# Optimization experiments

Hardware: AMD Instinct MI355X
Metric: run time of the kernel (lower is better)

## Reference

```python
import jax, jax.numpy as jnp
import numpy as np

B, S, D, H = 4, 2048, 1024, 16
HD = D // H  # head_dim = 64


def setup_inputs() -> dict:
    key = jax.random.key(0)
    ks = jax.random.split(key, 9)
    s = 1.0 / np.sqrt(D)
    return {
        "x": jax.random.normal(ks[0], (B, S, D), dtype=jnp.float32),
        "wq": jax.random.uniform(ks[1], (D, D), jnp.float32, -s, s),
        "bq": jax.random.uniform(ks[2], (D,), jnp.float32, -s, s),
        "wk": jax.random.uniform(ks[3], (D, D), jnp.float32, -s, s),
        "bk": jax.random.uniform(ks[4], (D,), jnp.float32, -s, s),
        "wv": jax.random.uniform(ks[5], (D, D), jnp.float32, -s, s),
        "bv": jax.random.uniform(ks[6], (D,), jnp.float32, -s, s),
        "wo": jax.random.uniform(ks[7], (D, D), jnp.float32, -s, s),
        "bo": jax.random.uniform(ks[8], (D,), jnp.float32, -s, s),
    }


def reference(x, wq, bq, wk, bk, wv, bv, wo, bo):
    b, s, _ = x.shape
    # projections (torch Linear: y = x @ W.T + b)
    q = (x @ wq.T + bq).reshape(b, s, H, HD).transpose(0, 2, 1, 3)  # [B,H,S,HD]
    k = (x @ wk.T + bk).reshape(b, s, H, HD).transpose(0, 2, 1, 3)
    v = (x @ wv.T + bv).reshape(b, s, H, HD).transpose(0, 2, 1, 3)
    scores = jnp.einsum("bhqd,bhkd->bhqk", q, k) / jnp.sqrt(jnp.float32(HD))
    attn = jax.nn.softmax(scores, axis=-1)  # full [B,H,S,S] as in original
    ctx = jnp.einsum("bhqk,bhkd->bhqd", attn, v)
    ctx = ctx.transpose(0, 2, 1, 3).reshape(b, s, D)
    return ctx @ wo.T + bo
```

## Files before the change

kernel.cpp:

```cpp
#include <hip/hip_runtime.h>
#include <stdint.h>


typedef __bf16 bf16x8 __attribute__((ext_vector_type(8)));
typedef float f32x4 __attribute__((ext_vector_type(4)));
typedef float f32x16 __attribute__((ext_vector_type(16)));

__device__ __forceinline__ uint16_t f2bf(float f) {
  union { float f; uint32_t u; } c;
  c.f = f;
  uint32_t u = c.u + 0x7fffu + ((c.u >> 16) & 1u);
  return (uint16_t)(u >> 16);
}

__device__ __forceinline__ float exp2_hw(float x) {
#if defined(__has_builtin) && __has_builtin(__builtin_amdgcn_exp2f)
  return __builtin_amdgcn_exp2f(x);
#else
  return exp2f(x);
#endif
}

__device__ __forceinline__ uint32_t cvt_pk_bf16(float lo, float hi) {
  uint32_t r;
  asm("v_cvt_pk_bf16_f32 %0, %1, %2" : "=v"(r) : "v"(lo), "v"(hi));
  return r;
}

__device__ __forceinline__ void gload16(const void* g, void* l) {
  __builtin_amdgcn_global_load_lds(
      (const __attribute__((address_space(1))) uint32_t*)g,
      (__attribute__((address_space(3))) uint32_t*)l,
      16, 0, 0);
}

__global__ void cvt_f32_bf16(const float* __restrict__ in,
                             uint16_t* __restrict__ out, int n4) {
  int i = blockIdx.x * blockDim.x + threadIdx.x;
  if (i >= n4) return;
  float4 v = reinterpret_cast<const float4*>(in)[i];
  union { uint16_t u[4]; uint2 d; } o;
  o.u[0] = f2bf(v.x); o.u[1] = f2bf(v.y);
  o.u[2] = f2bf(v.z); o.u[3] = f2bf(v.w);
  reinterpret_cast<uint2*>(out)[i] = o.d;
}

template <int MODE>
__global__ __launch_bounds__(256, 2)
void gemm_nt(const uint16_t* __restrict__ A,
             const uint16_t* __restrict__ W0, const uint16_t* __restrict__ W1,
             const uint16_t* __restrict__ W2,
             const float* __restrict__ b0, const float* __restrict__ b1,
             const float* __restrict__ b2,
             uint16_t* __restrict__ oq, uint16_t* __restrict__ ok2,
             uint16_t* __restrict__ ovT, float* __restrict__ ofp) {
  __shared__ __align__(16) uint16_t Alds[2][128 * 32];
  __shared__ __align__(16) uint16_t Blds[2][128 * 32];

  const int tid = threadIdx.x;
  const int w = tid >> 6;
  const int l = tid & 63;
  const int wm = w >> 1, wn = w & 1;
  const int g = l >> 4, c16 = l & 15;
  const int brow = blockIdx.y * 128;
  const int bcol = blockIdx.x * 128;

  const uint16_t* Wsel = W0;
  const float* bsel = b0;
  if (MODE == 0) {
    const int which = bcol >> 10;
    Wsel = (which == 0) ? W0 : ((which == 1) ? W1 : W2);
    bsel = (which == 0) ? b0 : ((which == 1) ? b1 : b2);
  }
  const int bw = bcol & 1023;

  const int srow = l >> 2;
  const int scol = (l & 3) * 8;

  f32x4 acc[4][4];
#pragma unroll
  for (int i = 0; i < 4; ++i)
#pragma unroll
    for (int j = 0; j < 4; ++j) acc[i][j] = {0.f, 0.f, 0.f, 0.f};

#pragma unroll
  for (int i2 = 0; i2 < 2; ++i2) {
    const int c = 2 * w + i2;
    gload16(A + (size_t)(brow + c * 16 + srow) * 1024 + scol, &Alds[0][c * 512]);
    gload16(Wsel + (size_t)(bw + c * 16 + srow) * 1024 + scol, &Blds[0][c * 512]);
  }

  for (int kt = 0; kt < 32; ++kt) {
    __syncthreads();
    const int cur = kt & 1;
    if (kt + 1 < 32) {
      const int k0 = (kt + 1) * 32;
#pragma unroll
      for (int i2 = 0; i2 < 2; ++i2) {
        const int c = 2 * w + i2;
        gload16(A + (size_t)(brow + c * 16 + srow) * 1024 + k0 + scol,
                &Alds[cur ^ 1][c * 512]);
        gload16(Wsel + (size_t)(bw + c * 16 + srow) * 1024 + k0 + scol,
                &Blds[cur ^ 1][c * 512]);
      }
    }
    bf16x8 af[4], bfr[4];
#pragma unroll
    for (int i = 0; i < 4; ++i)
      af[i] = *reinterpret_cast<const bf16x8*>(
          &Alds[cur][(wm * 64 + i * 16 + c16) * 32 + g * 8]);
#pragma unroll
    for (int j = 0; j < 4; ++j)
      bfr[j] = *reinterpret_cast<const bf16x8*>(
          &Blds[cur][(wn * 64 + j * 16 + c16) * 32 + g * 8]);
#pragma unroll
    for (int i = 0; i < 4; ++i)
#pragma unroll
      for (int j = 0; j < 4; ++j)
        acc[i][j] = __builtin_amdgcn_mfma_f32_16x16x32_bf16(af[i], bfr[j],
                                                            acc[i][j], 0, 0, 0);
  }

#pragma unroll
  for (int i = 0; i < 4; ++i) {
#pragma unroll
    for (int j = 0; j < 4; ++j) {
      const int n = bcol + wn * 64 + j * 16 + c16;
      const int nn = n & 1023;
      const float bias = bsel[nn];
#pragma unroll
      for (int r = 0; r < 4; ++r) {
        const int m = brow + wm * 64 + i * 16 + g * 4 + r;
        const float val = acc[i][j][r] + bias;
        if (MODE == 0) {
          const int which = n >> 10;
          const int s = m & 2047, b = m >> 11;
          const int h = nn >> 6, hd = nn & 63;
          const size_t bh = (size_t)(b * 16 + h);
          if (which == 0)
            oq[(bh * 2048 + s) * 64 + hd] = f2bf(val * 0.18033688011112042f);
          else if (which == 1)
            ok2[(bh * 2048 + s) * 64 + hd] = f2bf(val);
          else
            ovT[(bh * 64 + hd) * 2048 + s] = f2bf(val);
        } else {
          ofp[(size_t)m * 1024 + n] = val;
        }
      }
    }
  }
}

__global__ __launch_bounds__(256, 2)
void attn_fwd(const uint16_t* __restrict__ Q, const uint16_t* __restrict__ K,
              const uint16_t* __restrict__ VT, uint16_t* __restrict__ CTX) {
  __shared__ __align__(16) uint16_t Klds[2][64 * 64];
  __shared__ __align__(16) uint16_t Vlds[2][64 * 64];

  const int tid = threadIdx.x;
  const int w = tid >> 6;
  const int l = tid & 63;
  const int hi = l >> 5, q5 = l & 31;
  const int bh = blockIdx.x;
  const int qb = blockIdx.y;
  const int qrow_base = qb * 256 + w * 64;

  const int kappa = (q5 & 3) | (((q5 >> 3) & 1) << 2) | (((q5 >> 2) & 1) << 3) |
                    ((q5 >> 4) << 4);

  bf16x8 qf[2][4];
#pragma unroll
  for (int grp = 0; grp < 2; ++grp) {
    const uint16_t* qp =
        Q + ((size_t)bh * 2048 + qrow_base + grp * 32 + q5) * 64 + 8 * hi;
#pragma unroll
    for (int ks = 0; ks < 4; ++ks)
      qf[grp][ks] = *reinterpret_cast<const bf16x8*>(qp + 16 * ks);
  }

  f32x16 ctx[2][2];
#pragma unroll
  for (int grp = 0; grp < 2; ++grp)
#pragma unroll
    for (int hb = 0; hb < 2; ++hb)
#pragma unroll
      for (int e = 0; e < 16; ++e) ctx[grp][hb][e] = 0.f;
  float M[2] = {-1024.0f, -1024.0f};
  float L[2] = {0.f, 0.f};

  auto stage = [&](int kt, int buf) {
#pragma unroll
    for (int i2 = 0; i2 < 2; ++i2) {
      const int c = 2 * w + i2;
      const int lb = c * 1024 + l * 16;
      const int row = lb >> 7;
      const int so = lb ^ ((row & 7) << 4);
      const int colel = (so & 127) >> 1;
      gload16(K + ((size_t)bh * 2048 + kt * 64 + row) * 64 + colel,
              &Klds[buf][c * 512]);
      gload16(VT + ((size_t)bh * 64 + row) * 2048 + kt * 64 + colel,
              &Vlds[buf][c * 512]);
    }
  };

  int koff[4], voff[2][2];
#pragma unroll
  for (int ks = 0; ks < 4; ++ks)
    koff[ks] = (32 * ks + 16 * hi) ^ ((kappa & 7) << 4);
#pragma unroll
  for (int half = 0; half < 2; ++half)
#pragma unroll
    for (int ks2 = 0; ks2 < 2; ++ks2)
      voff[half][ks2] = (half * 64 + 32 * ks2 + 16 * hi) ^ ((q5 & 7) << 4);

  stage(0, 0);

  for (int kt = 0; kt < 32; ++kt) {
    __syncthreads();
    const int cur = kt & 1;
    if (kt + 1 < 32) stage(kt + 1, cur ^ 1);
    const uint8_t* kb = reinterpret_cast<const uint8_t*>(&Klds[cur][0]);
    const uint8_t* vb = reinterpret_cast<const uint8_t*>(&Vlds[cur][0]);

#pragma unroll
    for (int half = 0; half < 2; ++half) {
      bf16x8 kf[4];
      const int krow = half * 32 + kappa;
#pragma unroll
      for (int ks = 0; ks < 4; ++ks)
        kf[ks] = *reinterpret_cast<const bf16x8*>(kb + krow * 128 + koff[ks]);
      bf16x8 vf[2][2];
#pragma unroll
      for (int hb = 0; hb < 2; ++hb) {
        const int vrow = 32 * hb + q5;
#pragma unroll
        for (int ks2 = 0; ks2 < 2; ++ks2)
          vf[hb][ks2] = *reinterpret_cast<const bf16x8*>(
              vb + vrow * 128 + voff[half][ks2]);
      }

#pragma unroll
      for (int grp = 0; grp < 2; ++grp) {
        const float negM = -M[grp];
        f32x16 sc;
#pragma unroll
        for (int e = 0; e < 16; ++e) sc[e] = negM;
        __builtin_amdgcn_s_setprio(1);
#pragma unroll
        for (int ks = 0; ks < 4; ++ks)
          sc = __builtin_amdgcn_mfma_f32_32x32x16_bf16(kf[ks], qf[grp][ks], sc,
                                                       0, 0, 0);
        __builtin_amdgcn_s_setprio(0);

        float m0 = fmaxf(fmaxf(sc[0], sc[1]), fmaxf(sc[2], sc[3]));
        float m1 = fmaxf(fmaxf(sc[4], sc[5]), fmaxf(sc[6], sc[7]));
        float m2 = fmaxf(fmaxf(sc[8], sc[9]), fmaxf(sc[10], sc[11]));
        float m3 = fmaxf(fmaxf(sc[12], sc[13]), fmaxf(sc[14], sc[15]));
        float mloc = fmaxf(fmaxf(m0, m1), fmaxf(m2, m3));
        mloc = fmaxf(mloc, __shfl_xor(mloc, 32));

        float p[16];
        if (__any(mloc > 8.0f)) {
          const float delta = fmaxf(mloc, 0.0f);
          const float corr = exp2_hw(-delta);
          M[grp] += delta;
          L[grp] *= corr;
#pragma unroll
          for (int hb = 0; hb < 2; ++hb)
#pragma unroll
            for (int e = 0; e < 16; ++e) ctx[grp][hb][e] *= corr;
#pragma unroll
          for (int e = 0; e < 16; ++e) p[e] = exp2_hw(sc[e] - delta);
        } else {
#pragma unroll
          for (int e = 0; e < 16; ++e) p[e] = exp2_hw(sc[e]);
        }

        L[grp] += ((p[0] + p[1]) + (p[2] + p[3])) +
                  ((p[4] + p[5]) + (p[6] + p[7])) +
                  ((p[8] + p[9]) + (p[10] + p[11])) +
                  ((p[12] + p[13]) + (p[14] + p[15]));

        union { uint32_t u[4]; bf16x8 v; } pa0, pa1;
        pa0.u[0] = cvt_pk_bf16(p[0], p[1]);
        pa0.u[1] = cvt_pk_bf16(p[2], p[3]);
        pa0.u[2] = cvt_pk_bf16(p[4], p[5]);
        pa0.u[3] = cvt_pk_bf16(p[6], p[7]);
        pa1.u[0] = cvt_pk_bf16(p[8], p[9]);
        pa1.u[1] = cvt_pk_bf16(p[10], p[11]);
        pa1.u[2] = cvt_pk_bf16(p[12], p[13]);
        pa1.u[3] = cvt_pk_bf16(p[14], p[15]);

        __builtin_amdgcn_s_setprio(1);
#pragma unroll
        for (int hb = 0; hb < 2; ++hb) {
          ctx[grp][hb] = __builtin_amdgcn_mfma_f32_32x32x16_bf16(
              vf[hb][0], pa0.v, ctx[grp][hb], 0, 0, 0);
          ctx[grp][hb] = __builtin_amdgcn_mfma_f32_32x32x16_bf16(
              vf[hb][1], pa1.v, ctx[grp][hb], 0, 0, 0);
        }
        __builtin_amdgcn_s_setprio(0);
      }
    }
  }

  const int b = bh >> 4, h = bh & 15;
#pragma unroll
  for (int grp = 0; grp < 2; ++grp) {
    float Lt = L[grp] + __shfl_xor(L[grp], 32);
    const float inv = 1.0f / Lt;
    const int s = qrow_base + grp * 32 + q5;
#pragma unroll
    for (int hb = 0; hb < 2; ++hb) {
#pragma unroll
      for (int t = 0; t < 4; ++t) {
        uint2 st;
        st.x = cvt_pk_bf16(ctx[grp][hb][4 * t] * inv,
                           ctx[grp][hb][4 * t + 1] * inv);
        st.y = cvt_pk_bf16(ctx[grp][hb][4 * t + 2] * inv,
                           ctx[grp][hb][4 * t + 3] * inv);
        *reinterpret_cast<uint2*>(
            &CTX[((size_t)b * 2048 + s) * 1024 + h * 64 + hb * 32 + t * 8 +
                 hi * 4]) = st;
      }
    }
  }
}

extern "C" void kernel_launch(void* const* d_in, const int* in_sizes, int n_in,
                              void* d_out, int out_size, void* d_ws,
                              size_t ws_size, hipStream_t stream) {
  (void)in_sizes; (void)n_in; (void)out_size; (void)ws_size;
  const float* x = (const float*)d_in[0];
  const float* wq = (const float*)d_in[1];
  const float* bq = (const float*)d_in[2];
  const float* wk = (const float*)d_in[3];
  const float* bk = (const float*)d_in[4];
  const float* wv = (const float*)d_in[5];
  const float* bv = (const float*)d_in[6];
  const float* wo = (const float*)d_in[7];
  const float* bo = (const float*)d_in[8];
  float* out = (float*)d_out;

  uint8_t* ws = (uint8_t*)d_ws;
  uint16_t* xb   = (uint16_t*)(ws + 0);
  uint16_t* wqb  = (uint16_t*)(ws + 16777216);
  uint16_t* wkb  = (uint16_t*)(ws + 16777216 + 2097152);
  uint16_t* wvb  = (uint16_t*)(ws + 16777216 + 2 * 2097152);
  uint16_t* wob  = (uint16_t*)(ws + 16777216 + 3 * 2097152);
  uint16_t* qws  = (uint16_t*)(ws + 25165824);
  uint16_t* kws  = (uint16_t*)(ws + 25165824 + 16777216);
  uint16_t* vtws = (uint16_t*)(ws + 25165824 + 2 * 16777216);
  uint16_t* ctxw = (uint16_t*)(ws + 25165824 + 3 * 16777216);

  cvt_f32_bf16<<<8192, 256, 0, stream>>>(x, xb, 2097152);
  cvt_f32_bf16<<<1024, 256, 0, stream>>>(wq, wqb, 262144);
  cvt_f32_bf16<<<1024, 256, 0, stream>>>(wk, wkb, 262144);
  cvt_f32_bf16<<<1024, 256, 0, stream>>>(wv, wvb, 262144);
  cvt_f32_bf16<<<1024, 256, 0, stream>>>(wo, wob, 262144);

  gemm_nt<0><<<dim3(24, 64), 256, 0, stream>>>(
      xb, wqb, wkb, wvb, bq, bk, bv, qws, kws, vtws, nullptr);
  attn_fwd<<<dim3(64, 8), 256, 0, stream>>>(qws, kws, vtws, ctxw);
  gemm_nt<1><<<dim3(8, 64), 256, 0, stream>>>(
      ctxw, wob, nullptr, nullptr, bo, nullptr, nullptr, nullptr, nullptr,
      nullptr, out);
}
```

Baseline: 234.8 us.

## Process full 64-key tile per query group with one softmax rescale

Reorders the attention inner loop so each query group computes scores for both 32-key halves before a single max/rescale/exp step, instead of per half. This halves the number of max reductions, cross-lane shuffles, __any checks and potential ctx rescales per tile, and keeps the negated running max in a persistent vector instead of re-broadcasting it. The cost is more live registers (two score tiles plus extra P fragments) and K/V fragments reloaded from LDS per group rather than shared across groups, which could raise LDS traffic or pressure occupancy.

```diff
diff --git a/kernel.cpp b/kernel.cpp
--- a/kernel.cpp
+++ b/kernel.cpp
@@ -187,6 +187,11 @@
       for (int e = 0; e < 16; ++e) ctx[grp][hb][e] = 0.f;
   float M[2] = {-1024.0f, -1024.0f};
   float L[2] = {0.f, 0.f};
+  f32x16 negMv[2];
+#pragma unroll
+  for (int grp = 0; grp < 2; ++grp)
+#pragma unroll
+    for (int e = 0; e < 16; ++e) negMv[grp][e] = 1024.0f;
 
   auto stage = [&](int kt, int buf) {
 #pragma unroll
@@ -223,84 +228,134 @@
     const uint8_t* vb = reinterpret_cast<const uint8_t*>(&Vlds[cur][0]);
 
 #pragma unroll
-    for (int half = 0; half < 2; ++half) {
-      bf16x8 kf[4];
-      const int krow = half * 32 + kappa;
-#pragma unroll
-      for (int ks = 0; ks < 4; ++ks)
-        kf[ks] = *reinterpret_cast<const bf16x8*>(kb + krow * 128 + koff[ks]);
-      bf16x8 vf[2][2];
+    for (int grp = 0; grp < 2; ++grp) {
+      f32x16 scA, scB;
+      {
+        bf16x8 kf[4];
+#pragma unroll
+        for (int ks = 0; ks < 4; ++ks)
+          kf[ks] = *reinterpret_cast<const bf16x8*>(
+              kb + kappa * 128 + koff[ks]);
+        __builtin_amdgcn_s_setprio(1);
+        scA = __builtin_amdgcn_mfma_f32_32x32x16_bf16(kf[0], qf[grp][0],
+                                                      negMv[grp], 0, 0, 0);
+        scA = __builtin_amdgcn_mfma_f32_32x32x16_bf16(kf[1], qf[grp][1], scA,
+                                                      0, 0, 0);
+        scA = __builtin_amdgcn_mfma_f32_32x32x16_bf16(kf[2], qf[grp][2], scA,
+                                                      0, 0, 0);
+        scA = __builtin_amdgcn_mfma_f32_32x32x16_bf16(kf[3], qf[grp][3], scA,
+                                                      0, 0, 0);
+        __builtin_amdgcn_s_setprio(0);
+      }
+      {
+        bf16x8 kf[4];
+        const int krow = 32 + kappa;
+#pragma unroll
+        for (int ks = 0; ks < 4; ++ks)
+          kf[ks] = *reinterpret_cast<const bf16x8*>(
+              kb + krow * 128 + koff[ks]);
+        __builtin_amdgcn_s_setprio(1);
+        scB = __builtin_amdgcn_mfma_f32_32x32x16_bf16(kf[0], qf[grp][0],
+                                                      negMv[grp], 0, 0, 0);
+        scB = __builtin_amdgcn_mfma_f32_32x32x16_bf16(kf[1], qf[grp][1], scB,
+                                                      0, 0, 0);
+        scB = __builtin_amdgcn_mfma_f32_32x32x16_bf16(kf[2], qf[grp][2], scB,
+                                                      0, 0, 0);
+        scB = __builtin_amdgcn_mfma_f32_32x32x16_bf16(kf[3], qf[grp][3], scB,
+                                                      0, 0, 0);
+        __builtin_amdgcn_s_setprio(0);
+      }
+
+      float a0 = fmaxf(fmaxf(scA[0], scA[1]), scA[2]);
+      float a1 = fmaxf(fmaxf(scA[3], scA[4]), scA[5]);
+      float a2 = fmaxf(fmaxf(scA[6], scA[7]), scA[8]);
+      float a3 = fmaxf(fmaxf(scA[9], scA[10]), scA[11]);
+      float a4 = fmaxf(fmaxf(scA[12], scA[13]), scA[14]);
+      float b0 = fmaxf(fmaxf(scB[0], scB[1]), scB[2]);
+      float b1 = fmaxf(fmaxf(scB[3], scB[4]), scB[5]);
+      float b2 = fmaxf(fmaxf(scB[6], scB[7]), scB[8]);
+      float b3 = fmaxf(fmaxf(scB[9], scB[10]), scB[11]);
+      float b4 = fmaxf(fmaxf(scB[12], scB[13]), scB[14]);
+      float t0 = fmaxf(fmaxf(a0, a1), a2);
+      float t1 = fmaxf(fmaxf(a3, a4), scA[15]);
+      float t2 = fmaxf(fmaxf(b0, b1), b2);
+      float t3 = fmaxf(fmaxf(b3, b4), scB[15]);
+      float mloc = fmaxf(fmaxf(t0, t1), fmaxf(t2, t3));
+      mloc = fmaxf(mloc, __shfl_xor(mloc, 32));
+
+      float pA[16], pB[16];
+      if (__any(mloc > 8.0f)) {
+        const float delta = fmaxf(mloc, 0.0f);
+        const float corr = exp2_hw(-delta);
+        M[grp] += delta;
+        const float nM = -M[grp];
+#pragma unroll
+        for (int e = 0; e < 16; ++e) negMv[grp][e] = nM;
+        L[grp] *= corr;
+#pragma unroll
+        for (int hb = 0; hb < 2; ++hb)
+#pragma unroll
+          for (int e = 0; e < 16; ++e) ctx[grp][hb][e] *= corr;
+#pragma unroll
+        for (int e = 0; e < 16; ++e) pA[e] = exp2_hw(scA[e] - delta);
+#pragma unroll
+        for (int e = 0; e < 16; ++e) pB[e] = exp2_hw(scB[e] - delta);
+      } else {
+#pragma unroll
+        for (int e = 0; e < 16; ++e) pA[e] = exp2_hw(scA[e]);
+#pragma unroll
+        for (int e = 0; e < 16; ++e) pB[e] = exp2_hw(scB[e]);
+      }
+
+      L[grp] += ((((pA[0] + pA[1]) + (pA[2] + pA[3])) +
+                  ((pA[4] + pA[5]) + (pA[6] + pA[7]))) +
+                 (((pA[8] + pA[9]) + (pA[10] + pA[11])) +
+                  ((pA[12] + pA[13]) + (pA[14] + pA[15])))) +
+                ((((pB[0] + pB[1]) + (pB[2] + pB[3])) +
+                  ((pB[4] + pB[5]) + (pB[6] + pB[7]))) +
+                 (((pB[8] + pB[9]) + (pB[10] + pB[11])) +
+                  ((pB[12] + pB[13]) + (pB[14] + pB[15]))));
+
+      union { uint32_t u[4]; bf16x8 v; } paA0, paA1, paB0, paB1;
+      paA0.u[0] = cvt_pk_bf16(pA[0], pA[1]);
+      paA0.u[1] = cvt_pk_bf16(pA[2], pA[3]);
+      paA0.u[2] = cvt_pk_bf16(pA[4], pA[5]);
+      paA0.u[3] = cvt_pk_bf16(pA[6], pA[7]);
+      paA1.u[0] = cvt_pk_bf16(pA[8], pA[9]);
+      paA1.u[1] = cvt_pk_bf16(pA[10], pA[11]);
+      paA1.u[2] = cvt_pk_bf16(pA[12], pA[13]);
+      paA1.u[3] = cvt_pk_bf16(pA[14], pA[15]);
+      paB0.u[0] = cvt_pk_bf16(pB[0], pB[1]);
+      paB0.u[1] = cvt_pk_bf16(pB[2], pB[3]);
+      paB0.u[2] = cvt_pk_bf16(pB[4], pB[5]);
+      paB0.u[3] = cvt_pk_bf16(pB[6], pB[7]);
+      paB1.u[0] = cvt_pk_bf16(pB[8], pB[9]);
+      paB1.u[1] = cvt_pk_bf16(pB[10], pB[11]);
+      paB1.u[2] = cvt_pk_bf16(pB[12], pB[13]);
+      paB1.u[3] = cvt_pk_bf16(pB[14], pB[15]);
+
+      __builtin_amdgcn_s_setprio(1);
 #pragma unroll
       for (int hb = 0; hb < 2; ++hb) {
         const int vrow = 32 * hb + q5;
-#pragma unroll
-        for (int ks2 = 0; ks2 < 2; ++ks2)
-          vf[hb][ks2] = *reinterpret_cast<const bf16x8*>(
-              vb + vrow * 128 + voff[half][ks2]);
-      }
-
-#pragma unroll
-      for (int grp = 0; grp < 2; ++grp) {
-        const float negM = -M[grp];
-        f32x16 sc;
-#pragma unroll
-        for (int e = 0; e < 16; ++e) sc[e] = negM;
-        __builtin_amdgcn_s_setprio(1);
-#pragma unroll
-        for (int ks = 0; ks < 4; ++ks)
-          sc = __builtin_amdgcn_mfma_f32_32x32x16_bf16(kf[ks], qf[grp][ks], sc,
-                                                       0, 0, 0);
-        __builtin_amdgcn_s_setprio(0);
-
-        float m0 = fmaxf(fmaxf(sc[0], sc[1]), fmaxf(sc[2], sc[3]));
-        float m1 = fmaxf(fmaxf(sc[4], sc[5]), fmaxf(sc[6], sc[7]));
-        float m2 = fmaxf(fmaxf(sc[8], sc[9]), fmaxf(sc[10], sc[11]));
-        float m3 = fmaxf(fmaxf(sc[12], sc[13]), fmaxf(sc[14], sc[15]));
-        float mloc = fmaxf(fmaxf(m0, m1), fmaxf(m2, m3));
-        mloc = fmaxf(mloc, __shfl_xor(mloc, 32));
-
-        float p[16];
-        if (__any(mloc > 8.0f)) {
-          const float delta = fmaxf(mloc, 0.0f);
-          const float corr = exp2_hw(-delta);
-          M[grp] += delta;
-          L[grp] *= corr;
-#pragma unroll
-          for (int hb = 0; hb < 2; ++hb)
-#pragma unroll
-            for (int e = 0; e < 16; ++e) ctx[grp][hb][e] *= corr;
-#pragma unroll
-          for (int e = 0; e < 16; ++e) p[e] = exp2_hw(sc[e] - delta);
-        } else {
-#pragma unroll
-          for (int e = 0; e < 16; ++e) p[e] = exp2_hw(sc[e]);
-        }
-
-        L[grp] += ((p[0] + p[1]) + (p[2] + p[3])) +
-                  ((p[4] + p[5]) + (p[6] + p[7])) +
-                  ((p[8] + p[9]) + (p[10] + p[11])) +
-                  ((p[12] + p[13]) + (p[14] + p[15]));
-
-        union { uint32_t u[4]; bf16x8 v; } pa0, pa1;
-        pa0.u[0] = cvt_pk_bf16(p[0], p[1]);
-        pa0.u[1] = cvt_pk_bf16(p[2], p[3]);
-        pa0.u[2] = cvt_pk_bf16(p[4], p[5]);
-        pa0.u[3] = cvt_pk_bf16(p[6], p[7]);
-        pa1.u[0] = cvt_pk_bf16(p[8], p[9]);
-        pa1.u[1] = cvt_pk_bf16(p[10], p[11]);
-        pa1.u[2] = cvt_pk_bf16(p[12], p[13]);
-        pa1.u[3] = cvt_pk_bf16(p[14], p[15]);
-
-        __builtin_amdgcn_s_setprio(1);
-#pragma unroll
-        for (int hb = 0; hb < 2; ++hb) {
-          ctx[grp][hb] = __builtin_amdgcn_mfma_f32_32x32x16_bf16(
-              vf[hb][0], pa0.v, ctx[grp][hb], 0, 0, 0);
-          ctx[grp][hb] = __builtin_amdgcn_mfma_f32_32x32x16_bf16(
-              vf[hb][1], pa1.v, ctx[grp][hb], 0, 0, 0);
-        }
-        __builtin_amdgcn_s_setprio(0);
-      }
+        const bf16x8 vA0 = *reinterpret_cast<const bf16x8*>(
+            vb + vrow * 128 + voff[0][0]);
+        const bf16x8 vA1 = *reinterpret_cast<const bf16x8*>(
+            vb + vrow * 128 + voff[0][1]);
+        const bf16x8 vB0 = *reinterpret_cast<const bf16x8*>(
+            vb + vrow * 128 + voff[1][0]);
+        const bf16x8 vB1 = *reinterpret_cast<const bf16x8*>(
+            vb + vrow * 128 + voff[1][1]);
+        ctx[grp][hb] = __builtin_amdgcn_mfma_f32_32x32x16_bf16(
+            vA0, paA0.v, ctx[grp][hb], 0, 0, 0);
+        ctx[grp][hb] = __builtin_amdgcn_mfma_f32_32x32x16_bf16(
+            vA1, paA1.v, ctx[grp][hb], 0, 0, 0);
+        ctx[grp][hb] = __builtin_amdgcn_mfma_f32_32x32x16_bf16(
+            vB0, paB0.v, ctx[grp][hb], 0, 0, 0);
+        ctx[grp][hb] = __builtin_amdgcn_mfma_f32_32x32x16_bf16(
+            vB1, paB1.v, ctx[grp][hb], 0, 0, 0);
+      }
+      __builtin_amdgcn_s_setprio(0);
     }
   }
 
```

After: 387.2 us. 64.9% more time.

## Load K and V fragments directly from global memory instead of LDS staging

Applied to the files above, without the earlier changes.

Removes the double-buffered LDS staging of K and V tiles and their barriers. Each wave now reads its MFMA fragments straight from global memory, with V loads placed inside the inner loop. The launch-bounds occupancy hint is also dropped. This gets rid of LDS traffic and __syncthreads, but every wave re-fetches the same K/V data from cache, and global-load latency is now exposed right before the MFMAs with no prefetch.

```diff
diff --git a/kernel.cpp b/kernel.cpp
--- a/kernel.cpp
+++ b/kernel.cpp
@@ -151,12 +151,9 @@
   }
 }
 
-__global__ __launch_bounds__(256, 2)
+__global__ __launch_bounds__(256)
 void attn_fwd(const uint16_t* __restrict__ Q, const uint16_t* __restrict__ K,
               const uint16_t* __restrict__ VT, uint16_t* __restrict__ CTX) {
-  __shared__ __align__(16) uint16_t Klds[2][64 * 64];
-  __shared__ __align__(16) uint16_t Vlds[2][64 * 64];
-
   const int tid = threadIdx.x;
   const int w = tid >> 6;
   const int l = tid & 63;
@@ -188,56 +185,18 @@
   float M[2] = {-1024.0f, -1024.0f};
   float L[2] = {0.f, 0.f};
 
-  auto stage = [&](int kt, int buf) {
-#pragma unroll
-    for (int i2 = 0; i2 < 2; ++i2) {
-      const int c = 2 * w + i2;
-      const int lb = c * 1024 + l * 16;
-      const int row = lb >> 7;
-      const int so = lb ^ ((row & 7) << 4);
-      const int colel = (so & 127) >> 1;
-      gload16(K + ((size_t)bh * 2048 + kt * 64 + row) * 64 + colel,
-              &Klds[buf][c * 512]);
-      gload16(VT + ((size_t)bh * 64 + row) * 2048 + kt * 64 + colel,
-              &Vlds[buf][c * 512]);
-    }
-  };
-
-  int koff[4], voff[2][2];
-#pragma unroll
-  for (int ks = 0; ks < 4; ++ks)
-    koff[ks] = (32 * ks + 16 * hi) ^ ((kappa & 7) << 4);
-#pragma unroll
-  for (int half = 0; half < 2; ++half)
-#pragma unroll
-    for (int ks2 = 0; ks2 < 2; ++ks2)
-      voff[half][ks2] = (half * 64 + 32 * ks2 + 16 * hi) ^ ((q5 & 7) << 4);
-
-  stage(0, 0);
+  const uint16_t* kbase = K + ((size_t)bh * 2048 + kappa) * 64 + 8 * hi;
+  const uint16_t* vbase0 = VT + ((size_t)bh * 64 + q5) * 2048 + 8 * hi;
+  const uint16_t* vbase1 = vbase0 + 32 * 2048;
 
   for (int kt = 0; kt < 32; ++kt) {
-    __syncthreads();
-    const int cur = kt & 1;
-    if (kt + 1 < 32) stage(kt + 1, cur ^ 1);
-    const uint8_t* kb = reinterpret_cast<const uint8_t*>(&Klds[cur][0]);
-    const uint8_t* vb = reinterpret_cast<const uint8_t*>(&Vlds[cur][0]);
-
 #pragma unroll
     for (int half = 0; half < 2; ++half) {
       bf16x8 kf[4];
-      const int krow = half * 32 + kappa;
+      const uint16_t* kp = kbase + (size_t)(kt * 64 + half * 32) * 64;
 #pragma unroll
       for (int ks = 0; ks < 4; ++ks)
-        kf[ks] = *reinterpret_cast<const bf16x8*>(kb + krow * 128 + koff[ks]);
-      bf16x8 vf[2][2];
-#pragma unroll
-      for (int hb = 0; hb < 2; ++hb) {
-        const int vrow = 32 * hb + q5;
-#pragma unroll
-        for (int ks2 = 0; ks2 < 2; ++ks2)
-          vf[hb][ks2] = *reinterpret_cast<const bf16x8*>(
-              vb + vrow * 128 + voff[half][ks2]);
-      }
+        kf[ks] = *reinterpret_cast<const bf16x8*>(kp + 16 * ks);
 
 #pragma unroll
       for (int grp = 0; grp < 2; ++grp) {
@@ -294,10 +253,14 @@
         __builtin_amdgcn_s_setprio(1);
 #pragma unroll
         for (int hb = 0; hb < 2; ++hb) {
+          const uint16_t* vp =
+              (hb ? vbase1 : vbase0) + kt * 64 + half * 32;
+          const bf16x8 v0 = *reinterpret_cast<const bf16x8*>(vp);
+          const bf16x8 v1 = *reinterpret_cast<const bf16x8*>(vp + 16);
           ctx[grp][hb] = __builtin_amdgcn_mfma_f32_32x32x16_bf16(
-              vf[hb][0], pa0.v, ctx[grp][hb], 0, 0, 0);
+              v0, pa0.v, ctx[grp][hb], 0, 0, 0);
           ctx[grp][hb] = __builtin_amdgcn_mfma_f32_32x32x16_bf16(
-              vf[hb][1], pa1.v, ctx[grp][hb], 0, 0, 0);
+              v1, pa1.v, ctx[grp][hb], 0, 0, 0);
         }
         __builtin_amdgcn_s_setprio(0);
       }
```

After: 344.6 us. 46.7% more time.
